# Performance work log

Hardware: AMD Instinct MI355X
Metric: run time of the kernel (lower is better)

## Reference

```python
import jax, jax.numpy as jnp
import numpy as np

ENC, DEC, ATT = 2048, 512, 512

def setup_inputs() -> dict:
    key = jax.random.key(0)
    ks = jax.random.split(key, 8)
    B, L = 64, 1024
    s1 = 1.0 / np.sqrt(ENC)
    s2 = 1.0 / np.sqrt(DEC)
    s3 = 1.0 / np.sqrt(ATT)
    return {
        "features": jax.random.normal(ks[0], (B, L, ENC), jnp.float32),
        "hidden_state": jax.random.normal(ks[1], (B, DEC), jnp.float32),
        "W1": jax.random.uniform(ks[2], (ENC, ATT), jnp.float32, -s1, s1),
        "b1": jax.random.uniform(ks[3], (ATT,), jnp.float32, -s1, s1),
        "W2": jax.random.uniform(ks[4], (DEC, ATT), jnp.float32, -s2, s2),
        "b2": jax.random.uniform(ks[5], (ATT,), jnp.float32, -s2, s2),
        "V": jax.random.uniform(ks[6], (ATT, 1), jnp.float32, -s3, s3),
        "bv": jax.random.uniform(ks[7], (1,), jnp.float32, -s3, s3),
    }

def reference(features, hidden_state, W1, b1, W2, b2, V, bv):
    # features: [B, L, ENC], hidden_state: [B, DEC]
    proj_f = jnp.einsum('ble,ea->bla', features, W1) + b1          # [B, L, A]
    proj_h = (hidden_state @ W2 + b2)[:, None, :]                  # [B, 1, A]
    attention_hidden = jnp.tanh(proj_f + proj_h)                   # [B, L, A]
    score = jnp.einsum('bla,ao->blo', attention_hidden, V) + bv    # [B, L, 1]
    attention_weights = jax.nn.softmax(score, axis=1)              # [B, L, 1]
    context_vector = jnp.sum(attention_weights * features, axis=1) # [B, ENC]
    return (context_vector, attention_weights)
```

## Files before the change

### kernel.cpp

```cpp
#include <hip/hip_runtime.h>
#include <stdint.h>


typedef float  f32x4 __attribute__((ext_vector_type(4)));
typedef short  s16x8 __attribute__((ext_vector_type(8)));
typedef unsigned short u16x8 __attribute__((ext_vector_type(8)));

#define AS_GLB __attribute__((address_space(1)))
#define AS_LDS __attribute__((address_space(3)))

__device__ __forceinline__ unsigned short f2bf(float f) {
    unsigned int u = __float_as_uint(f);
    u += 0x7fffu + ((u >> 16) & 1u);
    return (unsigned short)(u >> 16);
}

__device__ __forceinline__ float fast_tanh(float x) {
    return 1.0f - 2.0f / (__expf(2.0f * x) + 1.0f);
}

__global__ __launch_bounds__(256) void k_w1t(const float* __restrict__ W1,
                                             unsigned short* __restrict__ w1t) {
    __shared__ float tile[64][65];
    const int k0 = blockIdx.x * 64;
    const int n0 = blockIdx.y * 64;
    const int t = threadIdx.x, ty = t >> 6, tx = t & 63;
    #pragma unroll
    for (int i = ty; i < 64; i += 4)
        tile[i][tx] = W1[(size_t)(k0 + i) * 512 + n0 + tx];
    __syncthreads();
    #pragma unroll
    for (int i = ty; i < 64; i += 4)
        w1t[(size_t)(n0 + i) * 2048 + k0 + tx] = f2bf(tile[tx][i]);
}

__global__ __launch_bounds__(256) void k_projh(const float* __restrict__ hs,
                                               const float* __restrict__ W2,
                                               const float* __restrict__ b2,
                                               float* __restrict__ ph) {
    __shared__ float hsm[512];
    __shared__ float part[256];
    const int b = blockIdx.x, c0 = blockIdx.y * 128, t = threadIdx.x;
    hsm[t]       = hs[b * 512 + t];
    hsm[t + 256] = hs[b * 512 + t + 256];
    __syncthreads();
    const int j = c0 + (t & 127), half = t >> 7;
    float s = 0.f;
    const float* wp = W2 + (size_t)(half * 256) * 512 + j;
    const float* hp = hsm + half * 256;
    #pragma unroll 8
    for (int i = 0; i < 256; ++i) s += hp[i] * wp[(size_t)i * 512];
    part[t] = s;
    __syncthreads();
    if (t < 128) ph[b * 512 + j] = part[t] + part[t + 128] + b2[j];
}

__global__ __launch_bounds__(256, 2) void k_score(const float* __restrict__ feat,
                                                  const unsigned short* __restrict__ w1t,
                                                  const float* __restrict__ b1,
                                                  const float* __restrict__ ph,
                                                  const float* __restrict__ V,
                                                  float* __restrict__ score) {
    __shared__ __align__(16) unsigned short As[64 * 32];
    __shared__ __align__(16) unsigned short Bs[512 * 32];
    __shared__ float red[4][64];

    const int tid  = threadIdx.x;
    const int wave = tid >> 6, lane = tid & 63;
    const int quad = lane >> 4, l15 = lane & 15;
    const int m0 = blockIdx.x * 64;
    const int bb = m0 >> 10;

    const int am = tid >> 2, ac = tid & 3;
    const float* aptr = feat + (size_t)(m0 + am) * 2048 + ac * 8;
    const int asl = (am * 4 + (ac ^ ((am >> 1) & 3))) * 8;

    const int bn0 = wave * 128 + (lane >> 2);
    const int bc  = (lane & 3) ^ ((lane >> 3) & 3);
    const unsigned short* bptr = w1t + (size_t)bn0 * 2048 + bc * 8;

    f32x4 acc[4][8];
    const f32x4 zero = {0.f, 0.f, 0.f, 0.f};
    #pragma unroll
    for (int i = 0; i < 4; ++i)
        #pragma unroll
        for (int j = 0; j < 8; ++j) acc[i][j] = zero;

    f32x4 a0 = *(const f32x4*)aptr;
    f32x4 a1 = *(const f32x4*)(aptr + 4);

    for (int ks = 0; ks < 64; ++ks) {
        __syncthreads();
        u16x8 aw;
        aw[0] = f2bf(a0.x); aw[1] = f2bf(a0.y); aw[2] = f2bf(a0.z); aw[3] = f2bf(a0.w);
        aw[4] = f2bf(a1.x); aw[5] = f2bf(a1.y); aw[6] = f2bf(a1.z); aw[7] = f2bf(a1.w);
        *(u16x8*)(&As[asl]) = aw;
        const unsigned short* g = bptr + ks * 32;
        #pragma unroll
        for (int r = 0; r < 8; ++r) {
            __builtin_amdgcn_global_load_lds((const AS_GLB uint32_t*)(g + (size_t)r * 32768),
                                             (AS_LDS uint32_t*)(&Bs[(wave * 512 + r * 64) * 8]),
                                             16, 0, 0);
        }
        __syncthreads();

        if (ks < 63) {
            const float* ap = aptr + (ks + 1) * 32;
            a0 = *(const f32x4*)ap;
            a1 = *(const f32x4*)(ap + 4);
        }

        s16x8 af[4], bf[8];
        #pragma unroll
        for (int i = 0; i < 4; ++i) {
            const int m = i * 16 + l15;
            af[i] = *(const s16x8*)(&As[(m * 4 + (quad ^ ((m >> 1) & 3))) * 8]);
        }
        #pragma unroll
        for (int j = 0; j < 8; ++j) {
            const int n = wave * 128 + j * 16 + l15;
            bf[j] = *(const s16x8*)(&Bs[(n * 4 + (quad ^ ((n >> 1) & 3))) * 8]);
        }
        #pragma unroll
        for (int i = 0; i < 4; ++i)
            #pragma unroll
            for (int j = 0; j < 8; ++j)
                acc[i][j] = __builtin_amdgcn_mfma_f32_16x16x32_bf16(af[i], bf[j], acc[i][j], 0, 0, 0);
    }

    float ls[4][4];
    #pragma unroll
    for (int i = 0; i < 4; ++i)
        #pragma unroll
        for (int r = 0; r < 4; ++r) ls[i][r] = 0.f;
    #pragma unroll
    for (int j = 0; j < 8; ++j) {
        const int n = wave * 128 + j * 16 + l15;
        const float bias = b1[n] + ph[bb * 512 + n];
        const float vj = V[n];
        #pragma unroll
        for (int i = 0; i < 4; ++i)
            #pragma unroll
            for (int r = 0; r < 4; ++r)
                ls[i][r] += vj * fast_tanh(acc[i][j][r] + bias);
    }
    #pragma unroll
    for (int m = 1; m < 16; m <<= 1)
        #pragma unroll
        for (int i = 0; i < 4; ++i)
            #pragma unroll
            for (int r = 0; r < 4; ++r)
                ls[i][r] += __shfl_xor(ls[i][r], m, 64);
    if (l15 == 0) {
        #pragma unroll
        for (int i = 0; i < 4; ++i)
            #pragma unroll
            for (int r = 0; r < 4; ++r)
                red[wave][i * 16 + quad * 4 + r] = ls[i][r];
    }
    __syncthreads();
    if (tid < 64)
        score[m0 + tid] = red[0][tid] + red[1][tid] + red[2][tid] + red[3][tid];
}

__global__ __launch_bounds__(256) void k_softmax(const float* __restrict__ score,
                                                 float* __restrict__ wout,
                                                 float* __restrict__ ctx,
                                                 int zero_ctx) {
    __shared__ float sred[4];
    const int b = blockIdx.x, t = threadIdx.x;
    const int wave = t >> 6, lane = t & 63;
    float s[4];
    #pragma unroll
    for (int i = 0; i < 4; ++i) s[i] = score[b * 1024 + t + i * 256];
    float mx = fmaxf(fmaxf(s[0], s[1]), fmaxf(s[2], s[3]));
    #pragma unroll
    for (int m = 1; m < 64; m <<= 1) mx = fmaxf(mx, __shfl_xor(mx, m, 64));
    if (lane == 0) sred[wave] = mx;
    __syncthreads();
    mx = fmaxf(fmaxf(sred[0], sred[1]), fmaxf(sred[2], sred[3]));
    float e[4], sum = 0.f;
    #pragma unroll
    for (int i = 0; i < 4; ++i) { e[i] = __expf(s[i] - mx); sum += e[i]; }
    #pragma unroll
    for (int m = 1; m < 64; m <<= 1) sum += __shfl_xor(sum, m, 64);
    __syncthreads();
    if (lane == 0) sred[wave] = sum;
    __syncthreads();
    const float inv = 1.0f / (sred[0] + sred[1] + sred[2] + sred[3]);
    #pragma unroll
    for (int i = 0; i < 4; ++i) wout[b * 1024 + t + i * 256] = e[i] * inv;
    if (zero_ctx) {
        #pragma unroll
        for (int i = 0; i < 8; ++i) ctx[b * 2048 + t + i * 256] = 0.f;
    }
}

__global__ __launch_bounds__(256) void k_ctx_part(const float* __restrict__ feat,
                                                  const float* __restrict__ wgt,
                                                  float* __restrict__ part) {
    __shared__ float wl[128];
    const int b = blockIdx.x, lc = blockIdx.y, t = threadIdx.x;
    if (t < 128) wl[t] = wgt[b * 1024 + lc * 128 + t];
    __syncthreads();
    const float* fp = feat + ((size_t)b * 1024 + (size_t)lc * 128) * 2048 + t * 8;
    f32x4 a0 = {0.f, 0.f, 0.f, 0.f}, a1 = {0.f, 0.f, 0.f, 0.f};
    #pragma unroll 4
    for (int l = 0; l < 128; ++l) {
        const f32x4 f0 = *(const f32x4*)(fp + (size_t)l * 2048);
        const f32x4 f1 = *(const f32x4*)(fp + (size_t)l * 2048 + 4);
        const float w = wl[l];
        a0 += w * f0;
        a1 += w * f1;
    }
    float* pp = part + ((size_t)(b * 8 + lc)) * 2048 + t * 8;
    *(f32x4*)pp = a0;
    *(f32x4*)(pp + 4) = a1;
}

__global__ __launch_bounds__(256) void k_ctx_red(const float* __restrict__ part,
                                                 float* __restrict__ ctx) {
    const int b = blockIdx.x, t = threadIdx.x;
    const float* pp = part + (size_t)b * 8 * 2048 + t * 8;
    f32x4 s0 = {0.f, 0.f, 0.f, 0.f}, s1 = {0.f, 0.f, 0.f, 0.f};
    #pragma unroll
    for (int r = 0; r < 8; ++r) {
        s0 += *(const f32x4*)(pp + (size_t)r * 2048);
        s1 += *(const f32x4*)(pp + (size_t)r * 2048 + 4);
    }
    float* cp = ctx + b * 2048 + t * 8;
    *(f32x4*)cp = s0;
    *(f32x4*)(cp + 4) = s1;
}

__global__ __launch_bounds__(256) void k_ctx_atomic(const float* __restrict__ feat,
                                                    const float* __restrict__ wgt,
                                                    float* __restrict__ ctx) {
    __shared__ float wl[128];
    const int b = blockIdx.x, lc = blockIdx.y, t = threadIdx.x;
    if (t < 128) wl[t] = wgt[b * 1024 + lc * 128 + t];
    __syncthreads();
    const float* fp = feat + ((size_t)b * 1024 + (size_t)lc * 128) * 2048 + t * 8;
    f32x4 a0 = {0.f, 0.f, 0.f, 0.f}, a1 = {0.f, 0.f, 0.f, 0.f};
    #pragma unroll 4
    for (int l = 0; l < 128; ++l) {
        const f32x4 f0 = *(const f32x4*)(fp + (size_t)l * 2048);
        const f32x4 f1 = *(const f32x4*)(fp + (size_t)l * 2048 + 4);
        const float w = wl[l];
        a0 += w * f0;
        a1 += w * f1;
    }
    float* cp = ctx + b * 2048 + t * 8;
    atomicAdd(cp + 0, a0.x); atomicAdd(cp + 1, a0.y);
    atomicAdd(cp + 2, a0.z); atomicAdd(cp + 3, a0.w);
    atomicAdd(cp + 4, a1.x); atomicAdd(cp + 5, a1.y);
    atomicAdd(cp + 6, a1.z); atomicAdd(cp + 7, a1.w);
}

extern "C" void kernel_launch(void* const* d_in, const int* in_sizes, int n_in,
                              void* d_out, int out_size, void* d_ws, size_t ws_size,
                              hipStream_t stream) {
    const float* feat = (const float*)d_in[0];
    const float* hs   = (const float*)d_in[1];
    const float* W1   = (const float*)d_in[2];
    const float* b1   = (const float*)d_in[3];
    const float* W2   = (const float*)d_in[4];
    const float* b2   = (const float*)d_in[5];
    const float* V    = (const float*)d_in[6];

    const size_t OFF_PH    = 2u * 1024 * 1024;
    const size_t OFF_SCORE = OFF_PH + 128u * 1024;
    const size_t OFF_PART  = OFF_SCORE + 256u * 1024;
    const size_t NEED_PART = OFF_PART + (size_t)64 * 8 * 2048 * 4;

    unsigned short* w1t = (unsigned short*)d_ws;
    float* ph    = (float*)((char*)d_ws + OFF_PH);
    float* score = (float*)((char*)d_ws + OFF_SCORE);
    float* part  = (float*)((char*)d_ws + OFF_PART);

    float* ctx  = (float*)d_out;
    float* wout = ctx + 64 * 2048;

    const int use_part = (ws_size >= NEED_PART) ? 1 : 0;

    k_w1t    <<<dim3(32, 8), 256, 0, stream>>>(W1, w1t);
    k_projh  <<<dim3(64, 4), 256, 0, stream>>>(hs, W2, b2, ph);
    k_score  <<<1024,        256, 0, stream>>>(feat, w1t, b1, ph, V, score);
    k_softmax<<<64,          256, 0, stream>>>(score, wout, ctx, use_part ? 0 : 1);
    if (use_part) {
        k_ctx_part<<<dim3(64, 8), 256, 0, stream>>>(feat, wout, part);
        k_ctx_red <<<64,          256, 0, stream>>>(part, ctx);
    } else {
        k_ctx_atomic<<<dim3(64, 8), 256, 0, stream>>>(feat, wout, ctx);
    }
}
```

Baseline: 926.0 us.

## Load MFMA operands directly from global memory, bypassing LDS staging

The score GEMM kernel stops staging the feature tile and W1 tile in shared memory. Each lane now loads its MFMA fragments straight from global memory, which removes both per-step barriers and the LDS traffic. The fp32-to-bf16 conversion also switches to a cheaper packed round-half-up form in place of round-to-nearest-even. In exchange there is no operand reuse across waves: the feature rows are reloaded by all four waves, global accesses become strided 32-byte chunks per lane, and latency hiding now depends on the compiler's unroll-by-2 scheduling.

```diff
diff --git a/kernel.cpp b/kernel.cpp
--- a/kernel.cpp
+++ b/kernel.cpp
@@ -4,15 +4,17 @@
 
 typedef float  f32x4 __attribute__((ext_vector_type(4)));
 typedef short  s16x8 __attribute__((ext_vector_type(8)));
-typedef unsigned short u16x8 __attribute__((ext_vector_type(8)));
-
-#define AS_GLB __attribute__((address_space(1)))
-#define AS_LDS __attribute__((address_space(3)))
 
 __device__ __forceinline__ unsigned short f2bf(float f) {
     unsigned int u = __float_as_uint(f);
     u += 0x7fffu + ((u >> 16) & 1u);
     return (unsigned short)(u >> 16);
+}
+
+__device__ __forceinline__ unsigned int pk_bf2(float a, float b) {
+    unsigned int ua = __float_as_uint(a) + 0x8000u;
+    unsigned int ub = __float_as_uint(b) + 0x8000u;
+    return (ua >> 16) | (ub & 0xffff0000u);
 }
 
 __device__ __forceinline__ float fast_tanh(float x) {
@@ -61,8 +63,6 @@
                                                   const float* __restrict__ ph,
                                                   const float* __restrict__ V,
                                                   float* __restrict__ score) {
-    __shared__ __align__(16) unsigned short As[64 * 32];
-    __shared__ __align__(16) unsigned short Bs[512 * 32];
     __shared__ float red[4][64];
 
     const int tid  = threadIdx.x;
@@ -71,13 +71,8 @@
     const int m0 = blockIdx.x * 64;
     const int bb = m0 >> 10;
 
-    const int am = tid >> 2, ac = tid & 3;
-    const float* aptr = feat + (size_t)(m0 + am) * 2048 + ac * 8;
-    const int asl = (am * 4 + (ac ^ ((am >> 1) & 3))) * 8;
-
-    const int bn0 = wave * 128 + (lane >> 2);
-    const int bc  = (lane & 3) ^ ((lane >> 3) & 3);
-    const unsigned short* bptr = w1t + (size_t)bn0 * 2048 + bc * 8;
+    const float*          ap = feat + (size_t)(m0 + l15) * 2048 + quad * 8;
+    const unsigned short* bp = w1t  + (size_t)(wave * 128 + l15) * 2048 + quad * 8;
 
     f32x4 acc[4][8];
     const f32x4 zero = {0.f, 0.f, 0.f, 0.f};
@@ -86,46 +81,31 @@
         #pragma unroll
         for (int j = 0; j < 8; ++j) acc[i][j] = zero;
 
-    f32x4 a0 = *(const f32x4*)aptr;
-    f32x4 a1 = *(const f32x4*)(aptr + 4);
-
+    #pragma unroll 2
     for (int ks = 0; ks < 64; ++ks) {
-        __syncthreads();
-        u16x8 aw;
-        aw[0] = f2bf(a0.x); aw[1] = f2bf(a0.y); aw[2] = f2bf(a0.z); aw[3] = f2bf(a0.w);
-        aw[4] = f2bf(a1.x); aw[5] = f2bf(a1.y); aw[6] = f2bf(a1.z); aw[7] = f2bf(a1.w);
-        *(u16x8*)(&As[asl]) = aw;
-        const unsigned short* g = bptr + ks * 32;
-        #pragma unroll
-        for (int r = 0; r < 8; ++r) {
-            __builtin_amdgcn_global_load_lds((const AS_GLB uint32_t*)(g + (size_t)r * 32768),
-                                             (AS_LDS uint32_t*)(&Bs[(wave * 512 + r * 64) * 8]),
-                                             16, 0, 0);
+        const int k0 = ks * 32;
+        s16x8 bf[8];
+        #pragma unroll
+        for (int j = 0; j < 8; ++j)
+            bf[j] = *(const s16x8*)(bp + (size_t)j * 16 * 2048 + k0);
+        s16x8 abf[4];
+        #pragma unroll
+        for (int i = 0; i < 4; ++i) {
+            const float* a = ap + (size_t)i * 16 * 2048 + k0;
+            const f32x4 lo = *(const f32x4*)a;
+            const f32x4 hi = *(const f32x4*)(a + 4);
+            union { unsigned int u[4]; s16x8 v; } r;
+            r.u[0] = pk_bf2(lo.x, lo.y);
+            r.u[1] = pk_bf2(lo.z, lo.w);
+            r.u[2] = pk_bf2(hi.x, hi.y);
+            r.u[3] = pk_bf2(hi.z, hi.w);
+            abf[i] = r.v;
         }
-        __syncthreads();
-
-        if (ks < 63) {
-            const float* ap = aptr + (ks + 1) * 32;
-            a0 = *(const f32x4*)ap;
-            a1 = *(const f32x4*)(ap + 4);
-        }
-
-        s16x8 af[4], bf[8];
-        #pragma unroll
-        for (int i = 0; i < 4; ++i) {
-            const int m = i * 16 + l15;
-            af[i] = *(const s16x8*)(&As[(m * 4 + (quad ^ ((m >> 1) & 3))) * 8]);
-        }
-        #pragma unroll
-        for (int j = 0; j < 8; ++j) {
-            const int n = wave * 128 + j * 16 + l15;
-            bf[j] = *(const s16x8*)(&Bs[(n * 4 + (quad ^ ((n >> 1) & 3))) * 8]);
-        }
         #pragma unroll
         for (int i = 0; i < 4; ++i)
             #pragma unroll
             for (int j = 0; j < 8; ++j)
-                acc[i][j] = __builtin_amdgcn_mfma_f32_16x16x32_bf16(af[i], bf[j], acc[i][j], 0, 0, 0);
+                acc[i][j] = __builtin_amdgcn_mfma_f32_16x16x32_bf16(abf[i], bf[j], acc[i][j], 0, 0, 0);
     }
 
     float ls[4][4];
```

Result: slower. 1.203 ms (+29.9%).
